# Performance work log

Measured on AMD Instinct MI355X. Metric: run time of the kernel, lower is better.

## Reference

```python
import jax, jax.numpy as jnp
import numpy as np
from jax.scipy.special import logsumexp

OFFSET = 2.0
SIG_OFF = 1.0 - 1.0 / (1.0 + np.exp(-OFFSET))  # 1 - sigmoid(offset)
EPS = 1e-22  # matches Flow++ safe_log clamp


def safe_log(x):
    return jnp.log(jnp.clip(x, EPS))


def setup_inputs() -> dict:
    key = jax.random.key(0)
    ks = jax.random.split(key, 6)
    B, K, C, L = 16, 16, 64, 2048
    x_change = jax.random.normal(ks[0], (B, C, L), jnp.float32)
    a = jax.random.normal(ks[1], (B, C, L), jnp.float32)
    b = jax.random.normal(ks[2], (B, C, L), jnp.float32)
    pi = jax.random.normal(ks[3], (B, K, C, L), jnp.float32)
    mu = jax.random.normal(ks[4], (B, K, C, L), jnp.float32)
    s = jax.random.normal(ks[5], (B, K, C, L), jnp.float32) * 0.1
    sldj = jnp.zeros((B,), jnp.float32)
    return {"x_change": x_change, "a": a, "b": b, "pi": pi, "mu": mu, "s": s, "sldj": sldj}


def reference(x_change, a, b, pi, mu, s, sldj):
    # Mixture-of-logistics coupling, forward direction (reverse=False, use_logmix=True).
    log_pi = jax.nn.log_softmax(pi, axis=1)                 # (B,K,C,L)
    z = (x_change[:, None] - mu) * jnp.exp(-s)              # (B,K,C,L) standardized
    # mixture_log_cdf: logsumexp_k [ log_pi_k + log sigmoid(z_k) ]
    log_cdf = logsumexp(log_pi + jax.nn.log_sigmoid(z), axis=1)   # (B,C,L)
    # mixture_log_pdf: logistic log-pdf = z - log_scale - 2*softplus(z)
    logistic_ldj = logsumexp(log_pi + z - s - 2.0 * jax.nn.softplus(z), axis=1)  # (B,C,L)
    u = jnp.exp(log_cdf)                                    # in (0,1)
    # sigmoid-inverse (logit) + its log-det: -log u - log(1-u)
    out = -safe_log(1.0 / u - 1.0)
    scale_ldj = -safe_log(u) - safe_log(1.0 - u)
    scale = jax.nn.sigmoid(a + OFFSET) + SIG_OFF
    B = x_change.shape[0]
    sldj = sldj + jnp.sum((logistic_ldj + scale_ldj + jnp.log(scale)).reshape(B, -1), axis=-1)
    out = (out + b) * scale
    return out, sldj
```

## Files before the change

### kernel.cpp

```cpp
#include <hip/hip_runtime.h>
#include <math.h>

constexpr int Bn   = 16;
constexpr int Kn   = 16;
constexpr int Cn   = 64;
constexpr int Ln   = 2048;
constexpr int CL   = Cn * Ln;
constexpr int Ntot = Bn * CL;
constexpr int VEC  = 4;
constexpr int TPB  = 256;
constexpr int EPB  = TPB * VEC;
constexpr int NBLK = Ntot / EPB;
constexpr int BLK_PER_B = CL / EPB;

constexpr float EPSF    = 1e-22f;
constexpr float SIG_OFF = 0.11920292202211755f;

__device__ __forceinline__ void lse_up(float v, float& m, float& s) {
    float nm = fmaxf(m, v);
    s = s * __expf(m - nm) + __expf(v - nm);
    m = nm;
}

__global__ __launch_bounds__(TPB) void flowpp_fwd(
    const float* __restrict__ x,  const float* __restrict__ a,
    const float* __restrict__ bb, const float* __restrict__ pi,
    const float* __restrict__ mu, const float* __restrict__ s,
    float* __restrict__ out, float* __restrict__ wsp)
{
    const int tid = threadIdx.x;
    const int e0  = blockIdx.x * EPB + tid * VEC;
    const int b   = blockIdx.x / BLK_PER_B;

    const float4 x4 = *(const float4*)(x + e0);
    const float xv[VEC] = {x4.x, x4.y, x4.z, x4.w};

    float m1[VEC], s1[VEC], m2[VEC], s2[VEC], m3[VEC], s3[VEC];
    #pragma unroll
    for (int i = 0; i < VEC; ++i) {
        m1[i] = m2[i] = m3[i] = -INFINITY;
        s1[i] = s2[i] = s3[i] = 0.f;
    }

    const int kbase = b * (Kn * CL) + (e0 - b * CL);

    #pragma unroll 4
    for (int k = 0; k < Kn; ++k) {
        const int off = kbase + k * CL;
        const float4 p4  = *(const float4*)(pi + off);
        const float4 mu4 = *(const float4*)(mu + off);
        const float4 sc4 = *(const float4*)(s  + off);
        const float pk[VEC] = {p4.x,  p4.y,  p4.z,  p4.w};
        const float mk[VEC] = {mu4.x, mu4.y, mu4.z, mu4.w};
        const float sk[VEC] = {sc4.x, sc4.y, sc4.z, sc4.w};
        #pragma unroll
        for (int i = 0; i < VEC; ++i) {
            float z  = (xv[i] - mk[i]) * __expf(-sk[i]);
            float az = fabsf(z);
            float t  = __logf(1.f + __expf(-az));
            float sp_pos = fmaxf(z, 0.f) + t;
            float sp_neg = sp_pos - z;
            lse_up(pk[i],                               m1[i], s1[i]);
            lse_up(pk[i] - sp_neg,                      m2[i], s2[i]);
            lse_up(pk[i] + z - sk[i] - 2.f * sp_pos,    m3[i], s3[i]);
        }
    }

    const float4 a4 = *(const float4*)(a  + e0);
    const float4 b4 = *(const float4*)(bb + e0);
    const float av[VEC] = {a4.x, a4.y, a4.z, a4.w};
    const float bv[VEC] = {b4.x, b4.y, b4.z, b4.w};

    float contrib = 0.f;
    float outv[VEC];
    #pragma unroll
    for (int i = 0; i < VEC; ++i) {
        float lse1     = m1[i] + __logf(s1[i]);
        float log_cdf  = m2[i] + __logf(s2[i]) - lse1;
        float ldj      = m3[i] + __logf(s3[i]) - lse1;
        float u        = __expf(log_cdf);
        float w        = 1.f / u - 1.f;
        float o        = -__logf(fmaxf(w, EPSF));
        float sc_ldj   = -__logf(fmaxf(u, EPSF)) - __logf(fmaxf(1.f - u, EPSF));
        float sc       = 1.f / (1.f + __expf(-(av[i] + 2.f))) + SIG_OFF;
        contrib += ldj + sc_ldj + __logf(sc);
        outv[i] = (o + bv[i]) * sc;
    }

    *(float4*)(out + e0) = make_float4(outv[0], outv[1], outv[2], outv[3]);

    #pragma unroll
    for (int off = 32; off; off >>= 1)
        contrib += __shfl_down(contrib, off);
    __shared__ float red[TPB / 64];
    if ((tid & 63) == 0) red[tid >> 6] = contrib;
    __syncthreads();
    if (tid == 0) {
        float t = red[0];
        #pragma unroll
        for (int wv = 1; wv < TPB / 64; ++wv) t += red[wv];
        wsp[blockIdx.x] = t;
    }
}

__global__ __launch_bounds__(64) void flowpp_sldj_reduce(
    const float* __restrict__ wsp, const float* __restrict__ sldj_in,
    float* __restrict__ sldj_out)
{
    const int b = blockIdx.x;
    const int t = threadIdx.x;
    float v = wsp[b * BLK_PER_B + t] + wsp[b * BLK_PER_B + 64 + t];
    #pragma unroll
    for (int off = 32; off; off >>= 1)
        v += __shfl_down(v, off);
    if (t == 0) sldj_out[b] = sldj_in[b] + v;
}

extern "C" void kernel_launch(void* const* d_in, const int* in_sizes, int n_in,
                              void* d_out, int out_size, void* d_ws, size_t ws_size,
                              hipStream_t stream) {
    const float* x    = (const float*)d_in[0];
    const float* a    = (const float*)d_in[1];
    const float* bb   = (const float*)d_in[2];
    const float* pi   = (const float*)d_in[3];
    const float* mu   = (const float*)d_in[4];
    const float* s    = (const float*)d_in[5];
    const float* sldj = (const float*)d_in[6];

    float* out      = (float*)d_out;
    float* sldj_out = (float*)d_out + Ntot;
    float* wsp      = (float*)d_ws;

    flowpp_fwd<<<NBLK, TPB, 0, stream>>>(x, a, bb, pi, mu, s, out, wsp);
    flowpp_sldj_reduce<<<Bn, 64, 0, stream>>>(wsp, sldj, sldj_out);
}
```

Measured before the change: 99.94 us.

## Replace online logsumexp with direct exp-sum mixture accumulation

Rewrites the per-component mixture math so that, instead of three running max-rescaled logsumexps, it accumulates plain sums of exp(pi), exp(pi)*sigmoid(z), exp(pi)*sigmoid(-z) and the pdf term. The output and log-det then come from logs of these sums, with 1-u computed as a separate sum. This removes several exp/log calls and max operations per component and should lower the transcendental ALU load. Without max subtraction it can overflow or underflow for large pi or z. That is safe for the standard-normal test inputs but not in general.

```diff
diff --git a/kernel.cpp b/kernel.cpp
--- a/kernel.cpp
+++ b/kernel.cpp
@@ -13,14 +13,8 @@
 constexpr int NBLK = Ntot / EPB;
 constexpr int BLK_PER_B = CL / EPB;
 
-constexpr float EPSF    = 1e-22f;
 constexpr float SIG_OFF = 0.11920292202211755f;
-
-__device__ __forceinline__ void lse_up(float v, float& m, float& s) {
-    float nm = fmaxf(m, v);
-    s = s * __expf(m - nm) + __expf(v - nm);
-    m = nm;
-}
+constexpr float TINY    = 1e-36f;
 
 __global__ __launch_bounds__(TPB) void flowpp_fwd(
     const float* __restrict__ x,  const float* __restrict__ a,
@@ -35,12 +29,9 @@
     const float4 x4 = *(const float4*)(x + e0);
     const float xv[VEC] = {x4.x, x4.y, x4.z, x4.w};
 
-    float m1[VEC], s1[VEC], m2[VEC], s2[VEC], m3[VEC], s3[VEC];
+    float S1[VEC], S2[VEC], S3[VEC], S4[VEC];
     #pragma unroll
-    for (int i = 0; i < VEC; ++i) {
-        m1[i] = m2[i] = m3[i] = -INFINITY;
-        s1[i] = s2[i] = s3[i] = 0.f;
-    }
+    for (int i = 0; i < VEC; ++i) { S1[i] = S2[i] = S3[i] = S4[i] = 0.f; }
 
     const int kbase = b * (Kn * CL) + (e0 - b * CL);
 
@@ -55,14 +46,18 @@
         const float sk[VEC] = {sc4.x, sc4.y, sc4.z, sc4.w};
         #pragma unroll
         for (int i = 0; i < VEC; ++i) {
-            float z  = (xv[i] - mk[i]) * __expf(-sk[i]);
-            float az = fabsf(z);
-            float t  = __logf(1.f + __expf(-az));
-            float sp_pos = fmaxf(z, 0.f) + t;
-            float sp_neg = sp_pos - z;
-            lse_up(pk[i],                               m1[i], s1[i]);
-            lse_up(pk[i] - sp_neg,                      m2[i], s2[i]);
-            lse_up(pk[i] + z - sk[i] - 2.f * sp_pos,    m3[i], s3[i]);
+            float es = __expf(-sk[i]);
+            float z  = (xv[i] - mk[i]) * es;
+            float ez = __expf(-z);
+            float g  = __builtin_amdgcn_rcpf(1.f + ez);
+            float e1 = __expf(pk[i]);
+            float t2 = e1 * g;
+            float t4 = t2 * ez;
+            float t3 = t4 * g * es;
+            S1[i] += e1;
+            S2[i] += t2;
+            S4[i] += t4;
+            S3[i] += t3;
         }
     }
 
@@ -75,16 +70,13 @@
     float outv[VEC];
     #pragma unroll
     for (int i = 0; i < VEC; ++i) {
-        float lse1     = m1[i] + __logf(s1[i]);
-        float log_cdf  = m2[i] + __logf(s2[i]) - lse1;
-        float ldj      = m3[i] + __logf(s3[i]) - lse1;
-        float u        = __expf(log_cdf);
-        float w        = 1.f / u - 1.f;
-        float o        = -__logf(fmaxf(w, EPSF));
-        float sc_ldj   = -__logf(fmaxf(u, EPSF)) - __logf(fmaxf(1.f - u, EPSF));
-        float sc       = 1.f / (1.f + __expf(-(av[i] + 2.f))) + SIG_OFF;
-        contrib += ldj + sc_ldj + __logf(sc);
-        outv[i] = (o + bv[i]) * sc;
+        float LA = __logf(fmaxf(S1[i], TINY));
+        float LB = __logf(fmaxf(S2[i], TINY));
+        float LC = __logf(fmaxf(S3[i], TINY));
+        float LD = __logf(fmaxf(S4[i], TINY));
+        float sc = __builtin_amdgcn_rcpf(1.f + __expf(-(av[i] + 2.f))) + SIG_OFF;
+        contrib += LC + LA - LB - LD + __logf(sc);
+        outv[i] = (LB - LD + bv[i]) * sc;
     }
 
     *(float4*)(out + e0) = make_float4(outv[0], outv[1], outv[2], outv[3]);
```

Result: faster. 88.04 us (-11.9%).
